# Kernel tuning notes

Hardware: AMD Instinct MI355X
Metric: run time of the kernel (lower is better)

Reference implementation:

```python
import jax, jax.numpy as jnp
import numpy as np

T = 96
CAP_MWH = 800.0
DP_RAMP = 65.0
DT = 0.25
ETA = float(np.sqrt(0.91))
L_MIN = 4
MAX_CHARGE_MWH = 1200.0
P_MAX = 195.0
N = 5 * T  # variable layout: [c, d, yc, yd, soc]
ITERS = 400  # fixed PDHG iterations (stand-in for SCS to eps=1e-5)

_VOFF = {'c': 0, 'd': 1, 'yc': 2, 'yd': 3, 'soc': 4}

def _idx(v, t):
    return _VOFF[v] * T + t

def _build_lp():
    G, h, A, b = [], [], [], []
    def ineq(pairs, rhs):
        r = np.zeros(N)
        for v, t, co in pairs:
            r[_idx(v, t)] += co
        G.append(r); h.append(rhs)
    def eq(pairs, rhs):
        r = np.zeros(N)
        for v, t, co in pairs:
            r[_idx(v, t)] += co
        A.append(r); b.append(rhs)
    for t in range(T):
        ineq([('c', t, 1.0)], P_MAX); ineq([('d', t, 1.0)], P_MAX)
        ineq([('c', t, -1.0)], 0.0); ineq([('d', t, -1.0)], 0.0)
        ineq([('yc', t, -1.0)], 0.0); ineq([('yc', t, 1.0)], 1.0)
        ineq([('yd', t, -1.0)], 0.0); ineq([('yd', t, 1.0)], 1.0)
        ineq([('soc', t, -1.0)], 0.0); ineq([('soc', t, 1.0)], CAP_MWH)
        ineq([('yc', t, 1.0), ('yd', t, 1.0)], 1.0)
        ineq([('c', t, 1.0), ('yc', t, -P_MAX)], 0.0)
        ineq([('d', t, 1.0), ('yd', t, -P_MAX)], 0.0)
    for t in range(1, T):
        ineq([('c', t, 1.0), ('c', t - 1, -1.0)], DP_RAMP)
        ineq([('c', t - 1, 1.0), ('c', t, -1.0)], DP_RAMP)
        ineq([('d', t, 1.0), ('d', t - 1, -1.0)], DP_RAMP)
        ineq([('d', t - 1, 1.0), ('d', t, -1.0)], DP_RAMP)
    for t in range(T - 1):
        ineq([('yc', t, 1.0), ('yd', t + 1, 1.0)], 1.0)
        ineq([('yd', t, 1.0), ('yc', t + 1, 1.0)], 1.0)
    for v in ('yc', 'yd'):
        for t in range(T):
            for k in range(1, L_MIN):
                if t + k >= T:
                    break
                if t > 0:
                    ineq([(v, t + k, -1.0), (v, t, 1.0), (v, t - 1, -1.0)], 0.0)
                else:
                    ineq([(v, t + k, -1.0), (v, t, 1.0)], 0.0)
    ineq([('c', t, DT) for t in range(T)], MAX_CHARGE_MWH)
    eq([('soc', 0, 1.0), ('c', 0, -ETA * DT), ('d', 0, DT / ETA)], 0.0)
    for t in range(1, T):
        eq([('soc', t, 1.0), ('soc', t - 1, -1.0), ('c', t, -ETA * DT), ('d', t, DT / ETA)], 0.0)
    eq([('soc', T - 1, 1.0)], 0.0)
    return np.array(G), np.array(h), np.array(A), np.array(b)

_G, _h, _A, _b = _build_lp()
_M_EQ = _A.shape[0]
_K_np = np.vstack([_A, _G]).astype(np.float32)
_kb_np = np.concatenate([_b, _h]).astype(np.float32)
_LNORM = float(np.linalg.norm(_K_np.astype(np.float64), 2))
TAU = np.float32(0.9 / _LNORM)
SIG = np.float32(0.9 / _LNORM)
K_MAT = jnp.asarray(_K_np)     # (M, N)
KB = jnp.asarray(_kb_np)       # (M,)


def _solve_one(price):
    # LP: min q^T x  s.t.  A x = b, G x <= h   (max price.(d-c)*DT)
    q = DT * jnp.concatenate([price, -price, jnp.zeros(3 * T, price.dtype)])
    def step(carry, _):
        x, y = carry
        x_new = x - TAU * (q + K_MAT.T @ y)
        x_bar = 2.0 * x_new - x
        y_new = y + SIG * (K_MAT @ x_bar - KB)
        # dual cone projection: equality duals free, inequality duals >= 0
        y_new = jnp.concatenate([y_new[:_M_EQ], jnp.maximum(y_new[_M_EQ:], 0.0)])
        return (x_new, y_new), None
    x0 = jnp.zeros(N, price.dtype)
    y0 = jnp.zeros(K_MAT.shape[0], price.dtype)
    (x, _), _ = jax.lax.scan(step, (x0, y0), None, length=ITERS)
    return x[:T], x[T:2 * T]  # (c, d)


def setup_inputs() -> dict:
    key = jax.random.key(0)
    # realistic-ish electricity prices: ~N(400, 100) CNY/MWh
    price = 400.0 + 100.0 * jax.random.normal(key, (256, T), dtype=jnp.float32)
    return {"price_pred": price}


def reference(price_pred):
    c, d = jax.vmap(_solve_one)(price_pred)  # each (B, 96)
    return c, d
```

## Files before the change

kernel.cpp:

```cpp
#include <hip/hip_runtime.h>
#include <math.h>


#define NITER 400
#define PITER 10
#define NY 1874
#define NX 520

__device__ __forceinline__ float wave_sum64(float v) {
  float r = v;
  int x;
  x = __builtin_amdgcn_update_dpp(0, __float_as_int(r), 0x111, 0xf, 0xf, true);
  r += __int_as_float(x);
  x = __builtin_amdgcn_update_dpp(0, __float_as_int(r), 0x112, 0xf, 0xf, true);
  r += __int_as_float(x);
  x = __builtin_amdgcn_update_dpp(0, __float_as_int(r), 0x114, 0xf, 0xf, true);
  r += __int_as_float(x);
  x = __builtin_amdgcn_update_dpp(0, __float_as_int(r), 0x118, 0xf, 0xf, true);
  r += __int_as_float(x);
  x = __builtin_amdgcn_update_dpp(0, __float_as_int(r), 0x142, 0xa, 0xf, true);
  r += __int_as_float(x);
  x = __builtin_amdgcn_update_dpp(0, __float_as_int(r), 0x143, 0xc, 0xf, true);
  r += __int_as_float(x);
  return __int_as_float(__builtin_amdgcn_readlane(__float_as_int(r), 63));
}

__global__ __launch_bounds__(512, 1)
void lp_solve_kernel(const float* __restrict__ price, float* __restrict__ out) {
  __shared__ float sy[NY];
  __shared__ float sxb[NX];
  __shared__ float s_red[8];

  const int tid = threadIdx.x, lane = tid & 63, wid = tid >> 6, bi = blockIdx.x;
  const double ETA_D = sqrt(0.91);
  const float cET = (float)(-(ETA_D * 0.25));
  const float cDE = (float)(0.25 / ETA_D);

  const bool colAct = (tid < 480);
  const int col = colAct ? tid : 479;
  const int vty = col / 96;
  const int t = col - 96 * vty;
  const int wX = 104 * vty + 4 + t;

  const int v01 = vty & 1;
  const int aBC = 1460 + 104 * v01 + t;
  const int aEQ = 1252 + t;
  const int aUM = 1667 + 104 * v01 + t;
  const float ce = v01 ? cDE : cET;
  const float ctc = v01 ? 0.f : 0.25f;

  const int yv = (vty >= 2) ? (vty - 2) : 0;
  const int bv = 624 * yv + t;
  const int bw = 624 * (1 - yv) + t;

  const float ce1 = (t <= 94) ? -1.f : 1.f;
  const int aBS = 1356 + t;

  const int tb = (wid == 0) ? lane : (64 + (lane & 31));
  const bool isBox = (wid == 0) || (wid == 1 && lane < 32);
  int er; bool eqRun, eqAct;
  if (wid == 1)      { er = (lane >= 32) ? lane - 32 : 0; eqRun = true; eqAct = (lane >= 32); }
  else if (wid == 5) { er = 32 + lane; eqRun = true; eqAct = true; }
  else if (wid == 7) { er = 96; eqRun = true; eqAct = (lane == 32); }
  else               { er = 0; eqRun = false; eqAct = false; }
  const float cEb = (er == 96) ? -1.f : 1.f;
  const bool mdRun = (wid >= 2) && (wid <= 4);
  const int mi0 = ((wid - 2) << 6) + lane;
  const bool mdAct = mdRun && (mi0 < 190);
  const int mi = mdAct ? mi0 : 189;
  const int mv = (mi >= 95) ? 1 : 0;
  const int mt = mi - 95 * mv;
  const int mx = 104 * (2 + mv) + mt;
  const int mw = 624 * mv + mt;
  const float cv2 = (mt <= 93) ? 1.f : 0.f;
  const float cv3 = (mt <= 92) ? 1.f : 0.f;
  const bool rRun = (wid == 5) || (wid == 6);
  const bool rAct = (wid == 5) || (wid == 6 && lane < 31);
  const int rt = (wid == 5) ? (1 + lane) : (65 + ((lane < 31) ? lane : 30));
  const bool sRun = (wid >= 6);
  const bool sAct = (wid == 6) || (wid == 7 && lane < 31);
  const int st = (wid == 6) ? lane : (64 + ((lane < 31) ? lane : 30));

  float xA = 0.f, qA = 0.f;
  float yb0=0,yb1=0,yb2=0,yb3=0,yb4=0,yb5=0,yb6=0,yb7=0,yb8=0,yb9=0,yb10=0,yb11=0,yb12=0;
  float ym1=0, ym2=0, ym3=0, yr0=0, yr1=0, yr2=0, yr3=0, ysw0=0, ysw1=0, yeq=0, ytc=0;

  auto gatherA = [&]() -> float {
    if (wid < 3) {
      float b = sy[aBC], e = sy[aEQ];
      float um = sy[aUM], up = sy[aUM + 1];
      float tc = sy[1872];
      return b + ce * e + um - up + ctc * tc;
    } else if (wid < 6) {
      float k1 = sy[bv + 3], k2 = sy[bv + 106], k3 = sy[bv + 209];
      float m0 = sy[bv + 316], m1 = sy[bv + 317];
      float bY = sy[bv + 420], s0 = sy[bv + 524], s1 = sy[bw + 523];
      return bY + s0 + s1 + (m0 - m1) - (k1 + k2 + k3);
    } else {
      float e0 = sy[aEQ], e1 = sy[aEQ + 1], bS = sy[aBS];
      return bS + e0 + ce1 * e1;
    }
  };

  float tauv = 0.f, sigv = 0.f;
  auto phaseBfull = [&](bool power) {
    const float sig = sigv;
    if (wid <= 1) {
      float c_ = sxb[4 + tb], d_ = sxb[108 + tb];
      float yc_ = sxb[212 + tb], yd_ = sxb[316 + tb], s_ = sxb[420 + tb];
      float v0,v1,v2,v3,v4,v5,v6,v7,v8,v9,v10,v11,v12;
      if (power) {
        v0=c_; v1=d_; v2=-c_; v3=-d_; v4=-yc_; v5=yc_; v6=-yd_; v7=yd_;
        v8=-s_; v9=s_; v10=yc_+yd_; v11=c_-195.f*yc_; v12=d_-195.f*yd_;
      } else {
        yb0  = fmaxf(yb0  + sig*(c_  - 195.f), 0.f);      v0 = yb0;
        yb1  = fmaxf(yb1  + sig*(d_  - 195.f), 0.f);      v1 = yb1;
        yb2  = fmaxf(yb2  - sig*c_,            0.f);      v2 = yb2;
        yb3  = fmaxf(yb3  - sig*d_,            0.f);      v3 = yb3;
        yb4  = fmaxf(yb4  - sig*yc_,           0.f);      v4 = yb4;
        yb5  = fmaxf(yb5  + sig*(yc_ - 1.f),   0.f);      v5 = yb5;
        yb6  = fmaxf(yb6  - sig*yd_,           0.f);      v6 = yb6;
        yb7  = fmaxf(yb7  + sig*(yd_ - 1.f),   0.f);      v7 = yb7;
        yb8  = fmaxf(yb8  - sig*s_,            0.f);      v8 = yb8;
        yb9  = fmaxf(yb9  + sig*(s_ - 800.f),  0.f);      v9 = yb9;
        yb10 = fmaxf(yb10 + sig*(yc_ + yd_ - 1.f), 0.f);  v10 = yb10;
        yb11 = fmaxf(yb11 + sig*(c_ - 195.f*yc_), 0.f);   v11 = yb11;
        yb12 = fmaxf(yb12 + sig*(d_ - 195.f*yd_), 0.f);   v12 = yb12;
      }
      if (isBox) {
        sy[1460 + tb] = v0 - v2 + v11;
        sy[1564 + tb] = v1 - v3 + v12;
        sy[420 + tb]  = -v4 + v5 + v10 - 195.f * v11;
        sy[1044 + tb] = -v6 + v7 + v10 - 195.f * v12;
        sy[1356 + tb] = -v8 + v9;
      }
    }
    if (mdRun) {
      float mp = sxb[mx + 3];
      float mc = sxb[mx + 4], m1v = sxb[mx + 5];
      float m2v = sxb[mx + 6], m3v = sxb[mx + 7];
      float base = mc - mp;
      float d1 = base - m1v, d2 = base - m2v, d3 = base - m3v;
      float o1, o2, o3;
      if (power) { o1 = d1; o2 = d2; o3 = d3; }
      else {
        ym1 = fmaxf(ym1 + sig * d1, 0.f); o1 = ym1;
        ym2 = fmaxf(ym2 + sig * d2, 0.f); o2 = ym2;
        ym3 = fmaxf(ym3 + sig * d3, 0.f); o3 = ym3;
      }
      if (mdAct) {
        sy[mw + 4]   = o1;
        sy[mw + 108] = o2;
        sy[mw + 212] = o3;
        sy[mw + 316] = o1 + cv2 * o2 + cv3 * o3;
      }
    }
    if (rRun) {
      float rcm = sxb[3 + rt], rc0 = sxb[4 + rt];
      float rdm = sxb[107 + rt], rd0 = sxb[108 + rt];
      float u0, u1, u2, u3;
      if (power) { u0 = rc0 - rcm; u1 = rcm - rc0; u2 = rd0 - rdm; u3 = rdm - rd0; }
      else {
        yr0 = fmaxf(yr0 + sig * (rc0 - rcm - 65.f), 0.f); u0 = yr0;
        yr1 = fmaxf(yr1 + sig * (rcm - rc0 - 65.f), 0.f); u1 = yr1;
        yr2 = fmaxf(yr2 + sig * (rd0 - rdm - 65.f), 0.f); u2 = yr2;
        yr3 = fmaxf(yr3 + sig * (rdm - rd0 - 65.f), 0.f); u3 = yr3;
      }
      if (rAct) { sy[1667 + rt] = u0 - u1; sy[1771 + rt] = u2 - u3; }
    }
    if (sRun) {
      float a0 = sxb[212 + st], a1 = sxb[213 + st];
      float b0 = sxb[316 + st], b1 = sxb[317 + st];
      float p0, p1;
      if (power) { p0 = a0 + b1; p1 = b0 + a1; }
      else {
        ysw0 = fmaxf(ysw0 + sig * (a0 + b1 - 1.f), 0.f); p0 = ysw0;
        ysw1 = fmaxf(ysw1 + sig * (b0 + a1 - 1.f), 0.f); p1 = ysw1;
      }
      if (sAct) { sy[524 + st] = p0; sy[1148 + st] = p1; }
    }
    if (eqRun) {
      float ep = sxb[419 + er], ecur = sxb[420 + er];
      float exc = sxb[4 + er], exd = sxb[108 + er];
      float dot = ecur - cEb * ep + cET * exc + cDE * exd;
      float ev;
      if (power) ev = dot;
      else { yeq += sig * dot; ev = yeq; }
      if (eqAct) sy[1252 + er] = ev;
    }
    if (wid == 7) {
      float ssum = sxb[4 + lane] + ((lane < 32) ? sxb[68 + lane] : 0.f);
      float tot = wave_sum64(ssum);
      float wv;
      if (power) wv = 0.25f * tot;
      else { ytc = fmaxf(ytc + sig * (0.25f * tot - 1200.f), 0.f); wv = ytc; }
      if (lane == 0) sy[1872] = wv;
    }
  };

  for (int i = tid; i < NY; i += 512) sy[i] = 0.f;
  for (int i = tid; i < NX; i += 512) sxb[i] = 0.f;
  __syncthreads();
  if (colAct) sxb[wX] = 1.f;
  __syncthreads();

  float lam2 = 1.f;
  for (int pit = 0; pit < PITER; ++pit) {
    phaseBfull(true);
    __syncthreads();
    float gA = gatherA();
    if (!colAct) gA = 0.f;
    float part = wave_sum64(gA * gA);
    if (lane == 0) s_red[wid] = part;
    __syncthreads();
    lam2 = sqrtf(s_red[0] + s_red[1] + s_red[2] + s_red[3]
               + s_red[4] + s_red[5] + s_red[6] + s_red[7]);
    float inv = 1.f / lam2;
    if (colAct) sxb[wX] = gA * inv;
    __syncthreads();
  }
  tauv = (float)(0.9 / sqrt((double)lam2));
  sigv = tauv;

  for (int i = tid; i < NY; i += 512) sy[i] = 0.f;
  if (tid < 96)       qA =  0.25f * price[bi * 96 + tid];
  else if (tid < 192) qA = -0.25f * price[bi * 96 + (tid - 96)];
  __syncthreads();

#pragma unroll 1
  for (int it = 0; it < NITER; ++it) {
    float gA = gatherA();
    if (colAct) {
      float xa = xA - tauv * (qA + gA);
      sxb[wX] = 2.f * xa - xA;
      xA = xa;
    }
    __syncthreads();
    phaseBfull(false);
    __syncthreads();
  }

  if (tid < 96)       out[bi * 96 + tid] = xA;
  else if (tid < 192) out[24576 + bi * 96 + (tid - 96)] = xA;
}

extern "C" void kernel_launch(void* const* d_in, const int* in_sizes, int n_in,
                              void* d_out, int out_size, void* d_ws, size_t ws_size,
                              hipStream_t stream) {
  const float* price = (const float*)d_in[0];
  float* outp = (float*)d_out;
  hipLaunchKernelGGL(lp_solve_kernel, dim3(256), dim3(512), 0, stream, price, outp);
}
```

Before: 259.5 us.

## Collapse per-problem LP solve from 8 waves to a single wavefront

```diff
diff --git a/kernel.cpp b/kernel.cpp
--- a/kernel.cpp
+++ b/kernel.cpp
@@ -25,109 +25,129 @@
   return __int_as_float(__builtin_amdgcn_readlane(__float_as_int(r), 63));
 }
 
-__global__ __launch_bounds__(512, 1)
+__global__ __launch_bounds__(64, 1)
 void lp_solve_kernel(const float* __restrict__ price, float* __restrict__ out) {
   __shared__ float sy[NY];
   __shared__ float sxb[NX];
-  __shared__ float s_red[8];
-
-  const int tid = threadIdx.x, lane = tid & 63, wid = tid >> 6, bi = blockIdx.x;
+
+  const int lane = threadIdx.x;
+  const int bi = blockIdx.x;
   const double ETA_D = sqrt(0.91);
   const float cET = (float)(-(ETA_D * 0.25));
   const float cDE = (float)(0.25 / ETA_D);
 
-  const bool colAct = (tid < 480);
-  const int col = colAct ? tid : 479;
-  const int vty = col / 96;
-  const int t = col - 96 * vty;
-  const int wX = 104 * vty + 4 + t;
-
-  const int v01 = vty & 1;
-  const int aBC = 1460 + 104 * v01 + t;
-  const int aEQ = 1252 + t;
-  const int aUM = 1667 + 104 * v01 + t;
-  const float ce = v01 ? cDE : cET;
-  const float ctc = v01 ? 0.f : 0.25f;
-
-  const int yv = (vty >= 2) ? (vty - 2) : 0;
-  const int bv = 624 * yv + t;
-  const int bw = 624 * (1 - yv) + t;
-
-  const float ce1 = (t <= 94) ? -1.f : 1.f;
-  const int aBS = 1356 + t;
-
-  const int tb = (wid == 0) ? lane : (64 + (lane & 31));
-  const bool isBox = (wid == 0) || (wid == 1 && lane < 32);
-  int er; bool eqRun, eqAct;
-  if (wid == 1)      { er = (lane >= 32) ? lane - 32 : 0; eqRun = true; eqAct = (lane >= 32); }
-  else if (wid == 5) { er = 32 + lane; eqRun = true; eqAct = true; }
-  else if (wid == 7) { er = 96; eqRun = true; eqAct = (lane == 32); }
-  else               { er = 0; eqRun = false; eqAct = false; }
-  const float cEb = (er == 96) ? -1.f : 1.f;
-  const bool mdRun = (wid >= 2) && (wid <= 4);
-  const int mi0 = ((wid - 2) << 6) + lane;
-  const bool mdAct = mdRun && (mi0 < 190);
-  const int mi = mdAct ? mi0 : 189;
-  const int mv = (mi >= 95) ? 1 : 0;
-  const int mt = mi - 95 * mv;
-  const int mx = 104 * (2 + mv) + mt;
-  const int mw = 624 * mv + mt;
-  const float cv2 = (mt <= 93) ? 1.f : 0.f;
-  const float cv3 = (mt <= 92) ? 1.f : 0.f;
-  const bool rRun = (wid == 5) || (wid == 6);
-  const bool rAct = (wid == 5) || (wid == 6 && lane < 31);
-  const int rt = (wid == 5) ? (1 + lane) : (65 + ((lane < 31) ? lane : 30));
-  const bool sRun = (wid >= 6);
-  const bool sAct = (wid == 6) || (wid == 7 && lane < 31);
-  const int st = (wid == 6) ? lane : (64 + ((lane < 31) ? lane : 30));
-
-  float xA = 0.f, qA = 0.f;
-  float yb0=0,yb1=0,yb2=0,yb3=0,yb4=0,yb5=0,yb6=0,yb7=0,yb8=0,yb9=0,yb10=0,yb11=0,yb12=0;
-  float ym1=0, ym2=0, ym3=0, yr0=0, yr1=0, yr2=0, yr3=0, ysw0=0, ysw1=0, yeq=0, ytc=0;
-
-  auto gatherA = [&]() -> float {
-    if (wid < 3) {
-      float b = sy[aBC], e = sy[aEQ];
-      float um = sy[aUM], up = sy[aUM + 1];
-      float tc = sy[1872];
-      return b + ce * e + um - up + ctc * tc;
-    } else if (wid < 6) {
-      float k1 = sy[bv + 3], k2 = sy[bv + 106], k3 = sy[bv + 209];
-      float m0 = sy[bv + 316], m1 = sy[bv + 317];
-      float bY = sy[bv + 420], s0 = sy[bv + 524], s1 = sy[bw + 523];
-      return bY + s0 + s1 + (m0 - m1) - (k1 + k2 + k3);
-    } else {
-      float e0 = sy[aEQ], e1 = sy[aEQ + 1], bS = sy[aBS];
-      return bS + e0 + ce1 * e1;
+  const int ts_[2] = { lane, (lane < 32) ? 64 + lane : 95 };
+  const bool actS1 = (lane < 32);
+
+  int mx_[3], mw_[3];
+  float cv2_[3], cv3_[3];
+  bool mact_[3];
+#pragma unroll
+  for (int k = 0; k < 3; ++k) {
+    int i = 64 * k + lane;
+    bool act = (i < 190);
+    mact_[k] = act;
+    int mi = act ? i : 189;
+    int mv = (mi >= 95) ? 1 : 0;
+    int mt = mi - 95 * mv;
+    mx_[k] = 104 * (2 + mv) + mt;
+    mw_[k] = 624 * mv + mt;
+    cv2_[k] = (mt <= 93) ? 1.f : 0.f;
+    cv3_[k] = (mt <= 92) ? 1.f : 0.f;
+  }
+  const int rt_[2] = { 1 + lane, 65 + ((lane < 31) ? lane : 30) };
+  const bool ract_[2] = { true, lane < 31 };
+  const int st_[2] = { lane, 64 + ((lane < 31) ? lane : 30) };
+  const bool sact_[2] = { true, lane < 31 };
+  const int er_[2] = { lane, 64 + ((lane < 32) ? lane : 32) };
+  const float cEb_[2] = { 1.f, (lane >= 32) ? -1.f : 1.f };
+  const bool eact_[2] = { true, lane <= 32 };
+  const int tb_[2] = { lane, 64 + (lane & 31) };
+  const bool bact_[2] = { true, lane < 32 };
+
+  float xA[10];
+  float q_[10];
+#pragma unroll
+  for (int j = 0; j < 10; ++j) { xA[j] = 0.f; q_[j] = 0.f; }
+  float yb[2][13], ym[3][3], yr[2][4], ysw[2][2], yeq[2];
+#pragma unroll
+  for (int s = 0; s < 2; ++s) {
+#pragma unroll
+    for (int j = 0; j < 13; ++j) yb[s][j] = 0.f;
+#pragma unroll
+    for (int j = 0; j < 4; ++j) yr[s][j] = 0.f;
+    ysw[s][0] = 0.f; ysw[s][1] = 0.f; yeq[s] = 0.f;
+  }
+#pragma unroll
+  for (int k = 0; k < 3; ++k) { ym[k][0] = 0.f; ym[k][1] = 0.f; ym[k][2] = 0.f; }
+  float ytc = 0.f;
+  float tcval = 0.f;
+  float tauv = 0.f, sigv = 0.f;
+
+  auto gatherAll = [&](float (&g)[10]) {
+#pragma unroll
+    for (int v01 = 0; v01 < 2; ++v01) {
+      const float ce = v01 ? cDE : cET;
+      const float ct = v01 ? 0.f : 0.25f;
+#pragma unroll
+      for (int s = 0; s < 2; ++s) {
+        const int t = ts_[s];
+        float b  = sy[1460 + 104 * v01 + t];
+        float e  = sy[1252 + t];
+        float um = sy[1667 + 104 * v01 + t];
+        float up = sy[1668 + 104 * v01 + t];
+        g[2 * v01 + s] = b + ce * e + um - up + ct * tcval;
+      }
+    }
+#pragma unroll
+    for (int yv = 0; yv < 2; ++yv) {
+#pragma unroll
+      for (int s = 0; s < 2; ++s) {
+        const int bv = 624 * yv + ts_[s];
+        const int bw = 624 * (1 - yv) + ts_[s];
+        float k1 = sy[bv + 3], k2 = sy[bv + 106], k3 = sy[bv + 209];
+        float m0 = sy[bv + 316], m1 = sy[bv + 317];
+        float bY = sy[bv + 420], s0 = sy[bv + 524], s1 = sy[bw + 523];
+        g[4 + 2 * yv + s] = bY + s0 + s1 + (m0 - m1) - (k1 + k2 + k3);
+      }
+    }
+#pragma unroll
+    for (int s = 0; s < 2; ++s) {
+      const int t = ts_[s];
+      float e0 = sy[1252 + t], e1 = sy[1253 + t], bS = sy[1356 + t];
+      const float ce1 = (t <= 94) ? -1.f : 1.f;
+      g[8 + s] = bS + e0 + ce1 * e1;
     }
   };
 
-  float tauv = 0.f, sigv = 0.f;
-  auto phaseBfull = [&](bool power) {
+  auto phaseB = [&](bool power) {
     const float sig = sigv;
-    if (wid <= 1) {
+#pragma unroll
+    for (int s = 0; s < 2; ++s) {
+      const int tb = tb_[s];
       float c_ = sxb[4 + tb], d_ = sxb[108 + tb];
       float yc_ = sxb[212 + tb], yd_ = sxb[316 + tb], s_ = sxb[420 + tb];
-      float v0,v1,v2,v3,v4,v5,v6,v7,v8,v9,v10,v11,v12;
+      float v0, v1, v2, v3, v4, v5, v6, v7, v8, v9, v10, v11, v12;
       if (power) {
-        v0=c_; v1=d_; v2=-c_; v3=-d_; v4=-yc_; v5=yc_; v6=-yd_; v7=yd_;
-        v8=-s_; v9=s_; v10=yc_+yd_; v11=c_-195.f*yc_; v12=d_-195.f*yd_;
+        v0 = c_; v1 = d_; v2 = -c_; v3 = -d_; v4 = -yc_; v5 = yc_;
+        v6 = -yd_; v7 = yd_; v8 = -s_; v9 = s_; v10 = yc_ + yd_;
+        v11 = c_ - 195.f * yc_; v12 = d_ - 195.f * yd_;
       } else {
-        yb0  = fmaxf(yb0  + sig*(c_  - 195.f), 0.f);      v0 = yb0;
-        yb1  = fmaxf(yb1  + sig*(d_  - 195.f), 0.f);      v1 = yb1;
-        yb2  = fmaxf(yb2  - sig*c_,            0.f);      v2 = yb2;
-        yb3  = fmaxf(yb3  - sig*d_,            0.f);      v3 = yb3;
-        yb4  = fmaxf(yb4  - sig*yc_,           0.f);      v4 = yb4;
-        yb5  = fmaxf(yb5  + sig*(yc_ - 1.f),   0.f);      v5 = yb5;
-        yb6  = fmaxf(yb6  - sig*yd_,           0.f);      v6 = yb6;
-        yb7  = fmaxf(yb7  + sig*(yd_ - 1.f),   0.f);      v7 = yb7;
-        yb8  = fmaxf(yb8  - sig*s_,            0.f);      v8 = yb8;
-        yb9  = fmaxf(yb9  + sig*(s_ - 800.f),  0.f);      v9 = yb9;
-        yb10 = fmaxf(yb10 + sig*(yc_ + yd_ - 1.f), 0.f);  v10 = yb10;
-        yb11 = fmaxf(yb11 + sig*(c_ - 195.f*yc_), 0.f);   v11 = yb11;
-        yb12 = fmaxf(yb12 + sig*(d_ - 195.f*yd_), 0.f);   v12 = yb12;
-      }
-      if (isBox) {
+        yb[s][0]  = fmaxf(yb[s][0]  + sig * (c_  - 195.f), 0.f);      v0 = yb[s][0];
+        yb[s][1]  = fmaxf(yb[s][1]  + sig * (d_  - 195.f), 0.f);      v1 = yb[s][1];
+        yb[s][2]  = fmaxf(yb[s][2]  - sig * c_,            0.f);      v2 = yb[s][2];
+        yb[s][3]  = fmaxf(yb[s][3]  - sig * d_,            0.f);      v3 = yb[s][3];
+        yb[s][4]  = fmaxf(yb[s][4]  - sig * yc_,           0.f);      v4 = yb[s][4];
+        yb[s][5]  = fmaxf(yb[s][5]  + sig * (yc_ - 1.f),   0.f);      v5 = yb[s][5];
+        yb[s][6]  = fmaxf(yb[s][6]  - sig * yd_,           0.f);      v6 = yb[s][6];
+        yb[s][7]  = fmaxf(yb[s][7]  + sig * (yd_ - 1.f),   0.f);      v7 = yb[s][7];
+        yb[s][8]  = fmaxf(yb[s][8]  - sig * s_,            0.f);      v8 = yb[s][8];
+        yb[s][9]  = fmaxf(yb[s][9]  + sig * (s_ - 800.f),  0.f);      v9 = yb[s][9];
+        yb[s][10] = fmaxf(yb[s][10] + sig * (yc_ + yd_ - 1.f), 0.f);  v10 = yb[s][10];
+        yb[s][11] = fmaxf(yb[s][11] + sig * (c_ - 195.f * yc_), 0.f); v11 = yb[s][11];
+        yb[s][12] = fmaxf(yb[s][12] + sig * (d_ - 195.f * yd_), 0.f); v12 = yb[s][12];
+      }
+      if (bact_[s]) {
         sy[1460 + tb] = v0 - v2 + v11;
         sy[1564 + tb] = v1 - v3 + v12;
         sy[420 + tb]  = -v4 + v5 + v10 - 195.f * v11;
@@ -135,7 +155,9 @@
         sy[1356 + tb] = -v8 + v9;
       }
     }
-    if (mdRun) {
+#pragma unroll
+    for (int k = 0; k < 3; ++k) {
+      const int mx = mx_[k], mw = mw_[k];
       float mp = sxb[mx + 3];
       float mc = sxb[mx + 4], m1v = sxb[mx + 5];
       float m2v = sxb[mx + 6], m3v = sxb[mx + 7];
@@ -144,104 +166,134 @@
       float o1, o2, o3;
       if (power) { o1 = d1; o2 = d2; o3 = d3; }
       else {
-        ym1 = fmaxf(ym1 + sig * d1, 0.f); o1 = ym1;
-        ym2 = fmaxf(ym2 + sig * d2, 0.f); o2 = ym2;
-        ym3 = fmaxf(ym3 + sig * d3, 0.f); o3 = ym3;
-      }
-      if (mdAct) {
+        ym[k][0] = fmaxf(ym[k][0] + sig * d1, 0.f); o1 = ym[k][0];
+        ym[k][1] = fmaxf(ym[k][1] + sig * d2, 0.f); o2 = ym[k][1];
+        ym[k][2] = fmaxf(ym[k][2] + sig * d3, 0.f); o3 = ym[k][2];
+      }
+      if (mact_[k]) {
         sy[mw + 4]   = o1;
         sy[mw + 108] = o2;
         sy[mw + 212] = o3;
-        sy[mw + 316] = o1 + cv2 * o2 + cv3 * o3;
-      }
-    }
-    if (rRun) {
+        sy[mw + 316] = o1 + cv2_[k] * o2 + cv3_[k] * o3;
+      }
+    }
+#pragma unroll
+    for (int k = 0; k < 2; ++k) {
+      const int rt = rt_[k];
       float rcm = sxb[3 + rt], rc0 = sxb[4 + rt];
       float rdm = sxb[107 + rt], rd0 = sxb[108 + rt];
       float u0, u1, u2, u3;
       if (power) { u0 = rc0 - rcm; u1 = rcm - rc0; u2 = rd0 - rdm; u3 = rdm - rd0; }
       else {
-        yr0 = fmaxf(yr0 + sig * (rc0 - rcm - 65.f), 0.f); u0 = yr0;
-        yr1 = fmaxf(yr1 + sig * (rcm - rc0 - 65.f), 0.f); u1 = yr1;
-        yr2 = fmaxf(yr2 + sig * (rd0 - rdm - 65.f), 0.f); u2 = yr2;
-        yr3 = fmaxf(yr3 + sig * (rdm - rd0 - 65.f), 0.f); u3 = yr3;
-      }
-      if (rAct) { sy[1667 + rt] = u0 - u1; sy[1771 + rt] = u2 - u3; }
-    }
-    if (sRun) {
+        yr[k][0] = fmaxf(yr[k][0] + sig * (rc0 - rcm - 65.f), 0.f); u0 = yr[k][0];
+        yr[k][1] = fmaxf(yr[k][1] + sig * (rcm - rc0 - 65.f), 0.f); u1 = yr[k][1];
+        yr[k][2] = fmaxf(yr[k][2] + sig * (rd0 - rdm - 65.f), 0.f); u2 = yr[k][2];
+        yr[k][3] = fmaxf(yr[k][3] + sig * (rdm - rd0 - 65.f), 0.f); u3 = yr[k][3];
+      }
+      if (ract_[k]) { sy[1667 + rt] = u0 - u1; sy[1771 + rt] = u2 - u3; }
+    }
+#pragma unroll
+    for (int k = 0; k < 2; ++k) {
+      const int st = st_[k];
       float a0 = sxb[212 + st], a1 = sxb[213 + st];
       float b0 = sxb[316 + st], b1 = sxb[317 + st];
       float p0, p1;
       if (power) { p0 = a0 + b1; p1 = b0 + a1; }
       else {
-        ysw0 = fmaxf(ysw0 + sig * (a0 + b1 - 1.f), 0.f); p0 = ysw0;
-        ysw1 = fmaxf(ysw1 + sig * (b0 + a1 - 1.f), 0.f); p1 = ysw1;
-      }
-      if (sAct) { sy[524 + st] = p0; sy[1148 + st] = p1; }
-    }
-    if (eqRun) {
+        ysw[k][0] = fmaxf(ysw[k][0] + sig * (a0 + b1 - 1.f), 0.f); p0 = ysw[k][0];
+        ysw[k][1] = fmaxf(ysw[k][1] + sig * (b0 + a1 - 1.f), 0.f); p1 = ysw[k][1];
+      }
+      if (sact_[k]) { sy[524 + st] = p0; sy[1148 + st] = p1; }
+    }
+#pragma unroll
+    for (int k = 0; k < 2; ++k) {
+      const int er = er_[k];
       float ep = sxb[419 + er], ecur = sxb[420 + er];
       float exc = sxb[4 + er], exd = sxb[108 + er];
-      float dot = ecur - cEb * ep + cET * exc + cDE * exd;
+      float dot = ecur - cEb_[k] * ep + cET * exc + cDE * exd;
       float ev;
       if (power) ev = dot;
-      else { yeq += sig * dot; ev = yeq; }
-      if (eqAct) sy[1252 + er] = ev;
-    }
-    if (wid == 7) {
+      else { yeq[k] += sig * dot; ev = yeq[k]; }
+      if (eact_[k]) sy[1252 + er] = ev;
+    }
+    {
       float ssum = sxb[4 + lane] + ((lane < 32) ? sxb[68 + lane] : 0.f);
       float tot = wave_sum64(ssum);
-      float wv;
-      if (power) wv = 0.25f * tot;
-      else { ytc = fmaxf(ytc + sig * (0.25f * tot - 1200.f), 0.f); wv = ytc; }
-      if (lane == 0) sy[1872] = wv;
+      if (power) tcval = 0.25f * tot;
+      else { ytc = fmaxf(ytc + sig * (0.25f * tot - 1200.f), 0.f); tcval = ytc; }
     }
   };
 
-  for (int i = tid; i < NY; i += 512) sy[i] = 0.f;
-  for (int i = tid; i < NX; i += 512) sxb[i] = 0.f;
+  for (int i = lane; i < NY; i += 64) sy[i] = 0.f;
+  for (int i = lane; i < NX; i += 64) sxb[i] = 0.f;
   __syncthreads();
-  if (colAct) sxb[wX] = 1.f;
+#pragma unroll
+  for (int j = 0; j < 10; ++j) {
+    const bool act = ((j & 1) == 0) || actS1;
+    if (act) sxb[104 * (j >> 1) + 4 + ts_[j & 1]] = 1.f;
+  }
   __syncthreads();
 
   float lam2 = 1.f;
   for (int pit = 0; pit < PITER; ++pit) {
-    phaseBfull(true);
+    phaseB(true);
     __syncthreads();
-    float gA = gatherA();
-    if (!colAct) gA = 0.f;
-    float part = wave_sum64(gA * gA);
-    if (lane == 0) s_red[wid] = part;
-    __syncthreads();
-    lam2 = sqrtf(s_red[0] + s_red[1] + s_red[2] + s_red[3]
-               + s_red[4] + s_red[5] + s_red[6] + s_red[7]);
+    float g[10];
+    gatherAll(g);
+    float part = 0.f;
+#pragma unroll
+    for (int j = 0; j < 10; ++j) {
+      const bool act = ((j & 1) == 0) || actS1;
+      if (act) part += g[j] * g[j];
+    }
+    lam2 = sqrtf(wave_sum64(part));
     float inv = 1.f / lam2;
-    if (colAct) sxb[wX] = gA * inv;
+#pragma unroll
+    for (int j = 0; j < 10; ++j) {
+      const bool act = ((j & 1) == 0) || actS1;
+      if (act) sxb[104 * (j >> 1) + 4 + ts_[j & 1]] = g[j] * inv;
+    }
     __syncthreads();
   }
   tauv = (float)(0.9 / sqrt((double)lam2));
   sigv = tauv;
 
-  for (int i = tid; i < NY; i += 512) sy[i] = 0.f;
-  if (tid < 96)       qA =  0.25f * price[bi * 96 + tid];
-  else if (tid < 192) qA = -0.25f * price[bi * 96 + (tid - 96)];
+  for (int i = lane; i < NY; i += 64) sy[i] = 0.f;
+  tcval = 0.f;
+  {
+    float p0 = price[bi * 96 + lane];
+    q_[0] = 0.25f * p0;
+    q_[2] = -0.25f * p0;
+    if (actS1) {
+      float p1 = price[bi * 96 + 64 + lane];
+      q_[1] = 0.25f * p1;
+      q_[3] = -0.25f * p1;
+    }
+  }
   __syncthreads();
 
 #pragma unroll 1
   for (int it = 0; it < NITER; ++it) {
-    float gA = gatherA();
-    if (colAct) {
-      float xa = xA - tauv * (qA + gA);
-      sxb[wX] = 2.f * xa - xA;
-      xA = xa;
+    float g[10];
+    gatherAll(g);
+#pragma unroll
+    for (int j = 0; j < 10; ++j) {
+      const bool act = ((j & 1) == 0) || actS1;
+      if (act) {
+        float xa = xA[j] - tauv * (q_[j] + g[j]);
+        sxb[104 * (j >> 1) + 4 + ts_[j & 1]] = 2.f * xa - xA[j];
+        xA[j] = xa;
+      }
     }
     __syncthreads();
-    phaseBfull(false);
+    phaseB(false);
     __syncthreads();
   }
 
-  if (tid < 96)       out[bi * 96 + tid] = xA;
-  else if (tid < 192) out[24576 + bi * 96 + (tid - 96)] = xA;
+  out[bi * 96 + lane] = xA[0];
+  if (actS1) out[bi * 96 + 64 + lane] = xA[1];
+  out[24576 + bi * 96 + lane] = xA[2];
+  if (actS1) out[24576 + bi * 96 + 64 + lane] = xA[3];
 }
 
 extern "C" void kernel_launch(void* const* d_in, const int* in_sizes, int n_in,
@@ -249,5 +301,5 @@
                               hipStream_t stream) {
   const float* price = (const float*)d_in[0];
   float* outp = (float*)d_out;
-  hipLaunchKernelGGL(lp_solve_kernel, dim3(256), dim3(512), 0, stream, price, outp);
+  hipLaunchKernelGGL(lp_solve_kernel, dim3(256), dim3(64), 0, stream, price, outp);
 }
```

Measured after the change: 568.0 us. 2.19x slower.
